# Optimization experiments

Measured on AMD Instinct MI355X. Metric: run time of the kernel, lower is better.

Reference implementation:

```python
import jax, jax.numpy as jnp
import numpy as np
import math

N_HEAD = 16
HEAD_QKV = 1024  # total qkv width; head_dim = HEAD_QKV // N_HEAD
WM_DECAY_LENGTH = 2048
WM_DECAY_RATE = 1.0
WM_ECHOIC = 16


def decay_weight_matrix(n):
    # power_law decay, faithful to get_decay_weight_matrix
    dl = WM_DECAY_LENGTH - WM_ECHOIC + 1
    nums = jnp.linspace(0.0, 1.0, dl)
    decay_values = 1.0 - jnp.power(nums, 1.0 / (np.e * WM_DECAY_RATE))
    decay_values = jnp.concatenate([jnp.ones(WM_ECHOIC - 1), decay_values])  # [WM_DECAY_LENGTH]
    decay_values = decay_values[:n]
    idx = jnp.arange(n)[:, None] - jnp.arange(n)[None, :]  # [n,n], negative above diag
    mat = decay_values[jnp.clip(idx, 0, n - 1)]
    return jnp.tril(mat).astype(jnp.float32)


def setup_inputs() -> dict:
    key = jax.random.key(0)
    k1, k2, k3 = jax.random.split(key, 3)
    B, T, C = 2, 2048, 1024
    x = jax.random.normal(k1, (B, T, C), dtype=jnp.float32)
    W_attn = jax.random.normal(k2, (C, 3 * HEAD_QKV), dtype=jnp.float32) * (1.0 / math.sqrt(C))
    W_proj = jax.random.normal(k3, (HEAD_QKV, C), dtype=jnp.float32) * (1.0 / math.sqrt(HEAD_QKV))
    return {"x": x, "W_attn": W_attn, "W_proj": W_proj}


def reference(x, W_attn, W_proj):
    B, T, C = x.shape
    hd = HEAD_QKV // N_HEAD
    qkv = x @ W_attn  # [B,T,3*HEAD_QKV]
    q, k, v = jnp.split(qkv, 3, axis=-1)
    # [B,T,HQKV] -> [B,H,T,hd]
    q = q.reshape(B, T, N_HEAD, hd).transpose(0, 2, 1, 3)
    k = k.reshape(B, T, N_HEAD, hd).transpose(0, 2, 1, 3)
    v = v.reshape(B, T, N_HEAD, hd).transpose(0, 2, 1, 3)
    att = jnp.einsum('bhqd,bhkd->bhqk', q, k) * (1.0 / math.sqrt(hd))
    causal = jnp.tril(jnp.ones((T, T), dtype=bool))
    att = jnp.where(causal, att, -jnp.inf)
    att = jax.nn.softmax(att, axis=-1)
    att = att * decay_weight_matrix(T)  # post-softmax multiplicative decay
    y = jnp.einsum('bhqk,bhkd->bhqd', att, v)
    y = y.transpose(0, 2, 1, 3).reshape(B, T, HEAD_QKV)
    return y @ W_proj
```

## Files before the change

kernel.cpp:

```cpp
#include <hip/hip_runtime.h>
#include <math.h>

#define B_  2
#define T_  2048
#define C_  1024
#define NH_ 16
#define HD_ 64
#define N3_ 3072

typedef float f32x4 __attribute__((ext_vector_type(4)));
typedef short bf16x8 __attribute__((ext_vector_type(8)));
typedef unsigned short u16;
typedef float f32x4_base __attribute__((ext_vector_type(4)));
typedef f32x4_base __attribute__((aligned(4))) f32x4u;

#define QSCALE 0.18033688011112042f

#if __has_builtin(__builtin_amdgcn_exp2f)
#define EXP2(x) __builtin_amdgcn_exp2f(x)
#else
#define EXP2(x) exp2f(x)
#endif

__device__ __forceinline__ u16 f2bf(float x) {
  unsigned int u = __builtin_bit_cast(unsigned int, x);
  u += 0x7FFFu + ((u >> 16) & 1u);
  return (u16)(u >> 16);
}

__device__ __forceinline__ unsigned int cvt_pk_bf16(float lo, float hi) {
  unsigned int r;
  asm("v_cvt_pk_bf16_f32 %0, %1, %2" : "=v"(r) : "v"(lo), "v"(hi));
  return r;
}

#define GLD16(g, l) __builtin_amdgcn_global_load_lds( \
    (__attribute__((address_space(1))) void*)(g), \
    (__attribute__((address_space(3))) void*)(l), 16, 0, 0)

__global__ __launch_bounds__(256) void prep_kernel(
    const float* __restrict__ x, u16* __restrict__ xb,
    const float* __restrict__ Wa, u16* __restrict__ WaT,
    const float* __restrict__ Wp, u16* __restrict__ WpT,
    float* __restrict__ decR)
{
  __shared__ float tile[32][33];
  const int bid = blockIdx.x;
  const int tid = threadIdx.x;
  if (bid < 4096) {
    int i = (bid * 256 + tid) * 4;
    float4 v = *(const float4*)(x + i);
    ushort4 o;
    o.x = f2bf(v.x); o.y = f2bf(v.y); o.z = f2bf(v.z); o.w = f2bf(v.w);
    *(ushort4*)(xb + i) = o;
  } else if (bid < 8192) {
    const float* in; u16* out; int Cc, c0, r0;
    if (bid < 7168) {
      int t = bid - 4096;
      in = Wa; out = WaT; Cc = N3_;
      c0 = (t % 96) * 32; r0 = (t / 96) * 32;
    } else {
      int t = bid - 7168;
      in = Wp; out = WpT; Cc = C_;
      c0 = (t % 32) * 32; r0 = (t / 32) * 32;
    }
    int tx = tid & 31, ty = tid >> 5;
#pragma unroll
    for (int rr = ty; rr < 32; rr += 8)
      tile[rr][tx] = in[(size_t)(r0 + rr) * Cc + c0 + tx];
    __syncthreads();
#pragma unroll
    for (int rr = ty; rr < 32; rr += 8)
      out[(size_t)(c0 + rr) * 1024 + r0 + tx] = f2bf(tile[tx][rr]);
  } else {
    int j = (bid - 8192) * 256 + tid;
    if (j < 4352) {
      int d = 2047 - j;
      float v = 1.0f;
      if (d >= 15) v = 1.0f - powf((float)(d - 15) * (1.0f / 2032.0f), 0.36787944117144233f);
      decR[j] = v;
    }
  }
}

__global__ void __launch_bounds__(512, 1) gemm256_kernel(
    const u16* __restrict__ A, const u16* __restrict__ Bt,
    u16* __restrict__ Cq, u16* __restrict__ Vt,
    int M, int N, int K)
{
  extern __shared__ char lds[];
  const int tid = threadIdx.x;
  const int lane = tid & 63;
  const int wave = tid >> 6;
  const int wm = wave >> 2;
  const int wn = wave & 3;
  const int quad = lane >> 4;
  const int l15 = lane & 15;
  const int nxb = N >> 8;
  const int orig = blockIdx.x;
  const int cpx = (int)gridDim.x >> 3;
  const int wg = (orig & 7) * cpx + (orig >> 3);
  const int m0 = (wg / nxb) << 8;
  const int n0 = (wg % nxb) << 8;

  f32x4 acc[8][4] = {};

  const int abase = wm * 16384;
  const int bbase = 65536 + (wn >> 1) * 16384;
  const int brow0 = (wn & 1) * 64;

#define HSTAGE(arr, rowbase, tile, ldsoff)                                       \
  {                                                                              \
    _Pragma("unroll")                                                            \
    for (int p = 0; p < 2; ++p) {                                                \
      int chunk = p * 8192 + tid * 16;                                           \
      int row = chunk >> 7;                                                      \
      int colb = (chunk & 127) ^ ((row & 7) << 4);                               \
      GLD16((const char*)((arr) + (size_t)((rowbase) + row) * K + (size_t)(tile) * 64) + colb, \
            lds + (ldsoff) + chunk);                                             \
    }                                                                            \
  }

#define PHASE(mg, buf, BLOAD, WAIT, STAGE_STMT)                                  \
  {                                                                              \
    if (WAIT) asm volatile("s_waitcnt vmcnt(4)" ::: "memory");                   \
    __builtin_amdgcn_s_barrier();                                                \
    __builtin_amdgcn_sched_barrier(0);                                           \
    STAGE_STMT;                                                                  \
    if (BLOAD) {                                                                 \
      _Pragma("unroll")                                                          \
      for (int n = 0; n < 4; ++n) {                                              \
        int rl = brow0 + n * 16 + l15;                                           \
        int msk = (rl & 7) << 4;                                                 \
        bfr[n][0] = *(const bf16x8*)(lds + bbase + (buf) * 32768 + rl * 128 +    \
                                     ((quad * 16) ^ msk));                       \
        bfr[n][1] = *(const bf16x8*)(lds + bbase + (buf) * 32768 + rl * 128 +    \
                                     ((64 + quad * 16) ^ msk));                  \
      }                                                                          \
    }                                                                            \
    bf16x8 af[2][2];                                                             \
    _Pragma("unroll")                                                            \
    for (int mm = 0; mm < 2; ++mm) {                                             \
      int rl = (mg) * 32 + mm * 16 + l15;                                        \
      int msk = (rl & 7) << 4;                                                   \
      af[mm][0] = *(const bf16x8*)(lds + abase + (buf) * 32768 + rl * 128 +      \
                                   ((quad * 16) ^ msk));                         \
      af[mm][1] = *(const bf16x8*)(lds + abase + (buf) * 32768 + rl * 128 +      \
                                   ((64 + quad * 16) ^ msk));                    \
    }                                                                            \
    __builtin_amdgcn_s_setprio(1);                                               \
    _Pragma("unroll")                                                            \
    for (int mm = 0; mm < 2; ++mm)                                               \
      _Pragma("unroll")                                                          \
      for (int n = 0; n < 4; ++n) {                                              \
        acc[(mg) * 2 + mm][n] = __builtin_amdgcn_mfma_f32_16x16x32_bf16(         \
            af[mm][0], bfr[n][0], acc[(mg) * 2 + mm][n], 0, 0, 0);               \
        acc[(mg) * 2 + mm][n] = __builtin_amdgcn_mfma_f32_16x16x32_bf16(         \
            af[mm][1], bfr[n][1], acc[(mg) * 2 + mm][n], 0, 0, 0);               \
      }                                                                          \
    __builtin_amdgcn_s_setprio(0);                                               \
  }

  bf16x8 bfr[4][2];

  HSTAGE(Bt, n0 + 0,   0, 65536 + 0);
  HSTAGE(Bt, n0 + 128, 0, 65536 + 16384);
  HSTAGE(A,  m0 + 0,   0, 0);
  HSTAGE(A,  m0 + 128, 0, 16384);
  HSTAGE(Bt, n0 + 0,   1, 65536 + 32768);
  HSTAGE(Bt, n0 + 128, 1, 65536 + 32768 + 16384);

  const int nt = K >> 6;
  const int tm = nt - 1;
  for (int j = 0; j < nt / 2; ++j) {
    const int t1 = 2 * j + 1, t2 = (2 * j + 2) & tm, t3 = (2 * j + 3) & tm;
    PHASE(0, 0, true,  true,  HSTAGE(A, m0 + 0,   t1, 32768));
    PHASE(1, 0, false, false, HSTAGE(A, m0 + 128, t1, 32768 + 16384));
    PHASE(2, 0, false, false, HSTAGE(Bt, n0 + 0,   t2, 65536));
    PHASE(3, 0, false, false, HSTAGE(Bt, n0 + 128, t2, 65536 + 16384));
    PHASE(0, 1, true,  true,  HSTAGE(A, m0 + 0,   t2, 0));
    PHASE(1, 1, false, false, HSTAGE(A, m0 + 128, t2, 16384));
    PHASE(2, 1, false, false, HSTAGE(Bt, n0 + 0,   t3, 65536 + 32768));
    PHASE(3, 1, false, false, HSTAGE(Bt, n0 + 128, t3, 65536 + 32768 + 16384));
  }
#undef PHASE
#undef HSTAGE

#pragma unroll
  for (int m = 0; m < 8; ++m) {
    int grow0 = m0 + wm * 128 + m * 16 + quad * 4;
#pragma unroll
    for (int n = 0; n < 4; ++n) {
      int gcol = n0 + wn * 64 + n * 16 + l15;
      f32x4 v = acc[m][n];
      int bb = grow0 >> 11, tt0 = grow0 & 2047;
      int which = gcol >> 10, rem = gcol & 1023;
      int hh = rem >> 6, dd = rem & 63;
      if (which < 2) {
#pragma unroll
        for (int r = 0; r < 4; ++r) {
          float ov = (which == 0) ? v[r] * QSCALE : v[r];
          Cq[((size_t)(which * 32 + bb * 16 + hh) * 2048 + tt0 + r) * 64 + dd] = f2bf(ov);
        }
      } else {
        ushort4 o;
        o.x = f2bf(v[0]); o.y = f2bf(v[1]); o.z = f2bf(v[2]); o.w = f2bf(v[3]);
        *(ushort4*)(Vt + ((size_t)(bb * 16 + hh) * 64 + dd) * 2048 + tt0) = o;
      }
    }
  }
}

__global__ __launch_bounds__(256, 3) void gemm128_kernel(
    const u16* __restrict__ A, const u16* __restrict__ Bt,
    float* __restrict__ Cf, int M, int N, int K)
{
  __shared__ char lds[49152];
  const int lane = threadIdx.x & 63;
  const int wave = threadIdx.x >> 6;
  const int nxb = N >> 7;
  const int orig = blockIdx.x;
  const int cpx = (int)gridDim.x >> 3;
  const int wg = (orig & 7) * cpx + (orig >> 3);
  const int m0 = (wg / nxb) << 7;
  const int n0 = (wg % nxb) << 7;
  const int wm = wave >> 1, wn = wave & 1;

  f32x4 acc[4][4] = {};

#define GSTAGE(buf, k0)                                                          \
  {                                                                              \
    _Pragma("unroll")                                                            \
    for (int c = 0; c < 2; ++c) {                                                \
      int chunk = wave * 2048 + c * 1024;                                        \
      int row = (chunk >> 6) + (lane >> 2);                                      \
      int wb = ((lane & 3) << 4) ^ ((row & 3) << 4);                             \
      GLD16((const char*)(A  + (size_t)(m0 + row) * K + (k0)) + wb,              \
            lds + (buf) * 16384 + chunk);                                        \
      GLD16((const char*)(Bt + (size_t)(n0 + row) * K + (k0)) + wb,              \
            lds + (buf) * 16384 + 8192 + chunk);                                 \
    }                                                                            \
  }

  const int nk = K >> 5;
  GSTAGE(0, 0);
  GSTAGE(1, 32);
  __syncthreads();

  for (int i = 0; i < nk; ++i) {
    if (i + 1 < nk) asm volatile("s_waitcnt vmcnt(4)" ::: "memory");
    else            asm volatile("s_waitcnt vmcnt(0)" ::: "memory");
    __builtin_amdgcn_s_barrier();
    __builtin_amdgcn_sched_barrier(0);
    if (i + 2 < nk) GSTAGE((i + 2) % 3, (i + 2) * 32);

    const char* base = lds + (i % 3) * 16384;
    bf16x8 af[4], bfr[4];
#pragma unroll
    for (int m = 0; m < 4; ++m) {
      int row = wm * 64 + m * 16 + (lane & 15);
      int wb = ((lane >> 4) << 4) ^ ((row & 3) << 4);
      af[m] = *(const bf16x8*)(base + row * 64 + wb);
    }
#pragma unroll
    for (int n = 0; n < 4; ++n) {
      int row = wn * 64 + n * 16 + (lane & 15);
      int wb = ((lane >> 4) << 4) ^ ((row & 3) << 4);
      bfr[n] = *(const bf16x8*)(base + 8192 + row * 64 + wb);
    }
    __builtin_amdgcn_s_setprio(1);
#pragma unroll
    for (int m = 0; m < 4; ++m)
#pragma unroll
      for (int n = 0; n < 4; ++n)
        acc[m][n] = __builtin_amdgcn_mfma_f32_16x16x32_bf16(af[m], bfr[n], acc[m][n], 0, 0, 0);
    __builtin_amdgcn_s_setprio(0);
  }

#pragma unroll
  for (int m = 0; m < 4; ++m) {
    int grow0 = m0 + wm * 64 + m * 16 + ((lane >> 4) << 2);
#pragma unroll
    for (int n = 0; n < 4; ++n) {
      int gcol = n0 + wn * 64 + n * 16 + (lane & 15);
      f32x4 v = acc[m][n];
#pragma unroll
      for (int r = 0; r < 4; ++r)
        Cf[(size_t)(grow0 + r) * N + gcol] = v[r];
    }
  }
#undef GSTAGE
}

__global__ __launch_bounds__(256, 2) void attn_kernel(
    const u16* __restrict__ qkb, const u16* __restrict__ vtg,
    const float* __restrict__ decR, u16* __restrict__ yb)
{
  __shared__ char klds[2][8192];
  __shared__ char vlds[2][8192];
  __shared__ u16 plds[64 * 76];

  const int lane = threadIdx.x & 63;
  const int wave = threadIdx.x >> 6;
  const int quad = lane >> 4;
  const int l15 = lane & 15;
  const int orig = blockIdx.x;
  const int xcd = orig & 7;
  const int bh = xcd * 4 + ((orig >> 3) & 3);
  const int x = orig >> 5;
  const int qtA = x;
  const int qtB = 31 - x;
  const int b = bh >> 4, h = bh & 15;

  const u16* Q   = qkb + (size_t)bh * T_ * HD_;
  const u16* Kg  = qkb + (size_t)(32 + bh) * T_ * HD_;
  const u16* VTg = vtg + (size_t)bh * HD_ * T_;

  const int wrowB = qtB * 64 + wave * 16;
  const int wrowA = qtA * 64 + wave * 16;
  const int qB = wrowB + l15;
  const int qA = wrowA + l15;
  const float* dpB = decR + (2047 - qB + quad * 4);
  const float* dpA = decR + (2047 - qA + quad * 4);

  bf16x8 qaB[2], qaA[2];
  { const u16* qp = Q + (size_t)qB * HD_ + quad * 8;
    qaB[0] = *(const bf16x8*)qp; qaB[1] = *(const bf16x8*)(qp + 32); }
  { const u16* qp = Q + (size_t)qA * HD_ + quad * 8;
    qaA[0] = *(const bf16x8*)qp; qaA[1] = *(const bf16x8*)(qp + 32); }

  f32x4 accB[4] = {}, accA[4] = {};
  float lsumB = 0.0f, lsumA = 0.0f;

#define ASTAGE(buf, kt)                                                          \
  {                                                                              \
    _Pragma("unroll")                                                            \
    for (int c = 0; c < 2; ++c) {                                                \
      int chunk = wave * 2048 + c * 1024;                                        \
      int row = (chunk >> 7) + (lane >> 3);                                      \
      int wb = ((lane & 7) << 4) ^ ((row & 7) << 4);                             \
      GLD16((const char*)(Kg + (size_t)((kt) * 64 + row) * HD_) + wb,            \
            klds[buf] + chunk);                                                  \
      GLD16((const char*)(VTg + (size_t)row * T_ + (kt) * 64) + wb,              \
            vlds[buf] + chunk);                                                  \
    }                                                                            \
  }

  const int twoA1 = 2 * qtA + 1;

  f32x4 dc[4], dn[4];
#pragma unroll
  for (int f = 0; f < 4; ++f) dn[f] = *(const f32x4u*)(dpB + f * 16);
  ASTAGE(0, 0);
  __syncthreads();

  for (int u = 0; u < 33; ++u) {
    const int kt   = (u <= twoA1) ? (u >> 1) : (u - qtA - 1);
    const int selA = (u <= twoA1) ? (u & 1) : 0;
    const int cur  = kt & 1;

#pragma unroll
    for (int f = 0; f < 4; ++f) dc[f] = dn[f];
    {
      const int u1 = u + 1;
      const int kt1   = (u1 <= twoA1) ? (u1 >> 1) : (u1 - qtA - 1);
      const int selA1 = (u1 <= twoA1) ? (u1 & 1) : 0;
      const float* dnp = (selA1 ? dpA : dpB) + kt1 * 64;
#pragma unroll
      for (int f = 0; f < 4; ++f) dn[f] = *(const f32x4u*)(dnp + f * 16);
    }

    asm volatile("s_waitcnt vmcnt(4)" ::: "memory");
    __builtin_amdgcn_s_barrier();
    __builtin_amdgcn_sched_barrier(0);
    if (!selA && kt < qtB) ASTAGE(cur ^ 1, kt + 1);

    bf16x8 kf[4][2];
#pragma unroll
    for (int f = 0; f < 4; ++f) {
      int krow = f * 16 + l15;
      int base = krow * 128;
      int msk = (krow & 7) << 4;
      kf[f][0] = *(const bf16x8*)(klds[cur] + base + ((quad * 16) ^ msk));
      kf[f][1] = *(const bf16x8*)(klds[cur] + base + ((64 + quad * 16) ^ msk));
    }

    const bf16x8 q0 = selA ? qaA[0] : qaB[0];
    const bf16x8 q1 = selA ? qaA[1] : qaB[1];
    f32x4 s[4];
    __builtin_amdgcn_s_setprio(1);
#pragma unroll
    for (int f = 0; f < 4; ++f) {
      f32x4 t = {};
      t = __builtin_amdgcn_mfma_f32_16x16x32_bf16(kf[f][0], q0, t, 0, 0, 0);
      t = __builtin_amdgcn_mfma_f32_16x16x32_bf16(kf[f][1], q1, t, 0, 0, 0);
      s[f] = t;
    }
    __builtin_amdgcn_s_setprio(0);

    const int qtsel = selA ? qtA : qtB;
    if (kt == qtsel) {
      const int qsel = selA ? qA : qB;
#pragma unroll
      for (int f = 0; f < 4; ++f) {
        int key0 = kt * 64 + f * 16 + quad * 4;
#pragma unroll
        for (int r = 0; r < 4; ++r)
          if (key0 + r > qsel) s[f][r] = -1e30f;
      }
    }

    float ls = 0.0f;
#pragma unroll
    for (int f = 0; f < 4; ++f) {
      f32x4 p;
#pragma unroll
      for (int r = 0; r < 4; ++r) p[r] = EXP2(s[f][r]);
      ls += (p[0] + p[1]) + (p[2] + p[3]);
      unsigned int w0 = cvt_pk_bf16(p[0] * dc[f][0], p[1] * dc[f][1]);
      unsigned int w1 = cvt_pk_bf16(p[2] * dc[f][2], p[3] * dc[f][3]);
      uint2 wv; wv.x = w0; wv.y = w1;
      *(uint2*)(plds + (size_t)(wave * 16 + l15) * 76 + f * 16 + quad * 4) = wv;
    }
    if (selA) lsumA += ls; else lsumB += ls;

    bf16x8 vf[4][2];
#pragma unroll
    for (int n = 0; n < 4; ++n) {
      int vrow = n * 16 + l15;
      int mskv = (vrow & 7) << 4;
#pragma unroll
      for (int ks = 0; ks < 2; ++ks)
        vf[n][ks] = *(const bf16x8*)(vlds[cur] + vrow * 128 + ((ks * 64 + quad * 16) ^ mskv));
    }

    bf16x8 pa0 = *(const bf16x8*)(plds + (size_t)(wave * 16 + l15) * 76 + quad * 8);
    bf16x8 pa1 = *(const bf16x8*)(plds + (size_t)(wave * 16 + l15) * 76 + 32 + quad * 8);
    __builtin_amdgcn_s_setprio(1);
    if (selA) {
#pragma unroll
      for (int n = 0; n < 4; ++n) {
        accA[n] = __builtin_amdgcn_mfma_f32_16x16x32_bf16(pa0, vf[n][0], accA[n], 0, 0, 0);
        accA[n] = __builtin_amdgcn_mfma_f32_16x16x32_bf16(pa1, vf[n][1], accA[n], 0, 0, 0);
      }
    } else {
#pragma unroll
      for (int n = 0; n < 4; ++n) {
        accB[n] = __builtin_amdgcn_mfma_f32_16x16x32_bf16(pa0, vf[n][0], accB[n], 0, 0, 0);
        accB[n] = __builtin_amdgcn_mfma_f32_16x16x32_bf16(pa1, vf[n][1], accB[n], 0, 0, 0);
      }
    }
    __builtin_amdgcn_s_setprio(0);
  }
#undef ASTAGE

  lsumB += __shfl_xor(lsumB, 16); lsumB += __shfl_xor(lsumB, 32);
  lsumA += __shfl_xor(lsumA, 16); lsumA += __shfl_xor(lsumA, 32);
  float rB[4], rA[4];
#pragma unroll
  for (int r = 0; r < 4; ++r) {
    rB[r] = 1.0f / __shfl(lsumB, quad * 4 + r, 16);
    rA[r] = 1.0f / __shfl(lsumA, quad * 4 + r, 16);
  }
#pragma unroll
  for (int n = 0; n < 4; ++n) {
    int d = h * 64 + n * 16 + l15;
#pragma unroll
    for (int r = 0; r < 4; ++r) {
      int tB = wrowB + quad * 4 + r;
      int tA = wrowA + quad * 4 + r;
      yb[((size_t)b * T_ + tB) * 1024 + d] = f2bf(accB[n][r] * rB[r]);
      yb[((size_t)b * T_ + tA) * 1024 + d] = f2bf(accA[n][r] * rA[r]);
    }
  }
}

extern "C" void kernel_launch(void* const* d_in, const int* in_sizes, int n_in,
                              void* d_out, int out_size, void* d_ws, size_t ws_size,
                              hipStream_t stream) {
  const float* x  = (const float*)d_in[0];
  const float* Wa = (const float*)d_in[1];
  const float* Wp = (const float*)d_in[2];
  float* out = (float*)d_out;
  char* ws = (char*)d_ws;

  u16*   xb    = (u16*)(ws + 0);
  u16*   WaT   = (u16*)(ws + 8388608);
  u16*   WpT   = (u16*)(ws + 14680064);
  u16*   qkb   = (u16*)(ws + 16777216);
  float* decR  = (float*)(ws + 33554432);
  u16*   VT    = (u16*)(ws + 41943040);
  u16*   yb    = xb;

  hipFuncSetAttribute((const void*)gemm256_kernel,
                      hipFuncAttributeMaxDynamicSharedMemorySize, 131072);

  prep_kernel<<<8209, 256, 0, stream>>>(x, xb, Wa, WaT, Wp, WpT, decR);
  gemm256_kernel<<<192, 512, 131072, stream>>>(xb, WaT, qkb, VT, B_ * T_, N3_, C_);
  attn_kernel<<<512, 256, 0, stream>>>(qkb, VT, decR, yb);
  gemm128_kernel<<<256, 256, 0, stream>>>(yb, WpT, out, B_ * T_, 1024, 1024);
}
```

Baseline: 101.2 us.

## Drop LDS K/V staging in attention; one query tile per block, direct global loads

Attention blocks no longer pair two query tiles, and K/V tiles are no longer staged through double-buffered LDS with async copies. Each wave now reads K and V^T fragments straight from global memory (relying on L2/cache reuse across the four waves). The grid doubles to 1024 blocks with heavier-tiles-first ordering and launch bounds rise to 4 blocks per SM for more occupancy. The cost is redundant global/L2 traffic per wave, the loss of prefetch overlap, and per-block load imbalance no longer evened out by pairing.

```diff
diff --git a/kernel.cpp b/kernel.cpp
--- a/kernel.cpp
+++ b/kernel.cpp
@@ -292,12 +292,10 @@
 #undef GSTAGE
 }
 
-__global__ __launch_bounds__(256, 2) void attn_kernel(
+__global__ __launch_bounds__(256, 4) void attn_kernel(
     const u16* __restrict__ qkb, const u16* __restrict__ vtg,
     const float* __restrict__ decR, u16* __restrict__ yb)
 {
-  __shared__ char klds[2][8192];
-  __shared__ char vlds[2][8192];
   __shared__ u16 plds[64 * 76];
 
   const int lane = threadIdx.x & 63;
@@ -305,172 +303,109 @@
   const int quad = lane >> 4;
   const int l15 = lane & 15;
   const int orig = blockIdx.x;
-  const int xcd = orig & 7;
-  const int bh = xcd * 4 + ((orig >> 3) & 3);
-  const int x = orig >> 5;
-  const int qtA = x;
-  const int qtB = 31 - x;
+  const int x = orig & 31;
+  const int bh = ((x & 7) << 2) + (x >> 3);
+  const int g = orig >> 5;
+  const int j3 = g >> 3;
+  const int g0 = g & 7;
+  const int qt = (3 - j3) * 8 + ((j3 & 1) ? (7 - g0) : g0);
   const int b = bh >> 4, h = bh & 15;
 
   const u16* Q   = qkb + (size_t)bh * T_ * HD_;
   const u16* Kg  = qkb + (size_t)(32 + bh) * T_ * HD_;
   const u16* VTg = vtg + (size_t)bh * HD_ * T_;
 
-  const int wrowB = qtB * 64 + wave * 16;
-  const int wrowA = qtA * 64 + wave * 16;
-  const int qB = wrowB + l15;
-  const int qA = wrowA + l15;
-  const float* dpB = decR + (2047 - qB + quad * 4);
-  const float* dpA = decR + (2047 - qA + quad * 4);
-
-  bf16x8 qaB[2], qaA[2];
-  { const u16* qp = Q + (size_t)qB * HD_ + quad * 8;
-    qaB[0] = *(const bf16x8*)qp; qaB[1] = *(const bf16x8*)(qp + 32); }
-  { const u16* qp = Q + (size_t)qA * HD_ + quad * 8;
-    qaA[0] = *(const bf16x8*)qp; qaA[1] = *(const bf16x8*)(qp + 32); }
-
-  f32x4 accB[4] = {}, accA[4] = {};
-  float lsumB = 0.0f, lsumA = 0.0f;
-
-#define ASTAGE(buf, kt)                                                          \
-  {                                                                              \
-    _Pragma("unroll")                                                            \
-    for (int c = 0; c < 2; ++c) {                                                \
-      int chunk = wave * 2048 + c * 1024;                                        \
-      int row = (chunk >> 7) + (lane >> 3);                                      \
-      int wb = ((lane & 7) << 4) ^ ((row & 7) << 4);                             \
-      GLD16((const char*)(Kg + (size_t)((kt) * 64 + row) * HD_) + wb,            \
-            klds[buf] + chunk);                                                  \
-      GLD16((const char*)(VTg + (size_t)row * T_ + (kt) * 64) + wb,              \
-            vlds[buf] + chunk);                                                  \
-    }                                                                            \
-  }
-
-  const int twoA1 = 2 * qtA + 1;
-
-  f32x4 dc[4], dn[4];
-#pragma unroll
-  for (int f = 0; f < 4; ++f) dn[f] = *(const f32x4u*)(dpB + f * 16);
-  ASTAGE(0, 0);
-  __syncthreads();
-
-  for (int u = 0; u < 33; ++u) {
-    const int kt   = (u <= twoA1) ? (u >> 1) : (u - qtA - 1);
-    const int selA = (u <= twoA1) ? (u & 1) : 0;
-    const int cur  = kt & 1;
-
-#pragma unroll
-    for (int f = 0; f < 4; ++f) dc[f] = dn[f];
-    {
-      const int u1 = u + 1;
-      const int kt1   = (u1 <= twoA1) ? (u1 >> 1) : (u1 - qtA - 1);
-      const int selA1 = (u1 <= twoA1) ? (u1 & 1) : 0;
-      const float* dnp = (selA1 ? dpA : dpB) + kt1 * 64;
-#pragma unroll
-      for (int f = 0; f < 4; ++f) dn[f] = *(const f32x4u*)(dnp + f * 16);
-    }
-
-    asm volatile("s_waitcnt vmcnt(4)" ::: "memory");
-    __builtin_amdgcn_s_barrier();
-    __builtin_amdgcn_sched_barrier(0);
-    if (!selA && kt < qtB) ASTAGE(cur ^ 1, kt + 1);
-
+  const int wrow = qt * 64 + wave * 16;
+  const int q = wrow + l15;
+  const float* dp = decR + (2047 - q + quad * 4);
+
+  bf16x8 qa[2];
+  { const u16* qp = Q + (size_t)q * HD_ + quad * 8;
+    qa[0] = *(const bf16x8*)qp; qa[1] = *(const bf16x8*)(qp + 32); }
+
+  f32x4 acc[4] = {};
+  float lsum = 0.0f;
+
+  for (int kt = 0; kt <= qt; ++kt) {
+    const u16* Kt = Kg + (size_t)(kt * 64) * HD_;
     bf16x8 kf[4][2];
 #pragma unroll
     for (int f = 0; f < 4; ++f) {
-      int krow = f * 16 + l15;
-      int base = krow * 128;
-      int msk = (krow & 7) << 4;
-      kf[f][0] = *(const bf16x8*)(klds[cur] + base + ((quad * 16) ^ msk));
-      kf[f][1] = *(const bf16x8*)(klds[cur] + base + ((64 + quad * 16) ^ msk));
-    }
-
-    const bf16x8 q0 = selA ? qaA[0] : qaB[0];
-    const bf16x8 q1 = selA ? qaA[1] : qaB[1];
+      const u16* kp = Kt + (size_t)(f * 16 + l15) * HD_ + quad * 8;
+      kf[f][0] = *(const bf16x8*)(kp);
+      kf[f][1] = *(const bf16x8*)(kp + 32);
+    }
+
+    f32x4 dc[4];
+    const float* dk = dp + kt * 64;
+#pragma unroll
+    for (int f = 0; f < 4; ++f) dc[f] = *(const f32x4u*)(dk + f * 16);
+
     f32x4 s[4];
     __builtin_amdgcn_s_setprio(1);
 #pragma unroll
     for (int f = 0; f < 4; ++f) {
       f32x4 t = {};
-      t = __builtin_amdgcn_mfma_f32_16x16x32_bf16(kf[f][0], q0, t, 0, 0, 0);
-      t = __builtin_amdgcn_mfma_f32_16x16x32_bf16(kf[f][1], q1, t, 0, 0, 0);
+      t = __builtin_amdgcn_mfma_f32_16x16x32_bf16(kf[f][0], qa[0], t, 0, 0, 0);
+      t = __builtin_amdgcn_mfma_f32_16x16x32_bf16(kf[f][1], qa[1], t, 0, 0, 0);
       s[f] = t;
     }
     __builtin_amdgcn_s_setprio(0);
 
-    const int qtsel = selA ? qtA : qtB;
-    if (kt == qtsel) {
-      const int qsel = selA ? qA : qB;
+    if (kt == qt) {
 #pragma unroll
       for (int f = 0; f < 4; ++f) {
         int key0 = kt * 64 + f * 16 + quad * 4;
 #pragma unroll
         for (int r = 0; r < 4; ++r)
-          if (key0 + r > qsel) s[f][r] = -1e30f;
+          if (key0 + r > q) s[f][r] = -1e30f;
       }
     }
 
-    float ls = 0.0f;
 #pragma unroll
     for (int f = 0; f < 4; ++f) {
       f32x4 p;
 #pragma unroll
       for (int r = 0; r < 4; ++r) p[r] = EXP2(s[f][r]);
-      ls += (p[0] + p[1]) + (p[2] + p[3]);
+      lsum += (p[0] + p[1]) + (p[2] + p[3]);
       unsigned int w0 = cvt_pk_bf16(p[0] * dc[f][0], p[1] * dc[f][1]);
       unsigned int w1 = cvt_pk_bf16(p[2] * dc[f][2], p[3] * dc[f][3]);
       uint2 wv; wv.x = w0; wv.y = w1;
       *(uint2*)(plds + (size_t)(wave * 16 + l15) * 76 + f * 16 + quad * 4) = wv;
     }
-    if (selA) lsumA += ls; else lsumB += ls;
 
     bf16x8 vf[4][2];
 #pragma unroll
     for (int n = 0; n < 4; ++n) {
-      int vrow = n * 16 + l15;
-      int mskv = (vrow & 7) << 4;
+      const u16* vp = VTg + (size_t)(n * 16 + l15) * T_ + kt * 64 + quad * 8;
 #pragma unroll
       for (int ks = 0; ks < 2; ++ks)
-        vf[n][ks] = *(const bf16x8*)(vlds[cur] + vrow * 128 + ((ks * 64 + quad * 16) ^ mskv));
+        vf[n][ks] = *(const bf16x8*)(vp + ks * 32);
     }
 
     bf16x8 pa0 = *(const bf16x8*)(plds + (size_t)(wave * 16 + l15) * 76 + quad * 8);
     bf16x8 pa1 = *(const bf16x8*)(plds + (size_t)(wave * 16 + l15) * 76 + 32 + quad * 8);
     __builtin_amdgcn_s_setprio(1);
-    if (selA) {
-#pragma unroll
-      for (int n = 0; n < 4; ++n) {
-        accA[n] = __builtin_amdgcn_mfma_f32_16x16x32_bf16(pa0, vf[n][0], accA[n], 0, 0, 0);
-        accA[n] = __builtin_amdgcn_mfma_f32_16x16x32_bf16(pa1, vf[n][1], accA[n], 0, 0, 0);
-      }
-    } else {
-#pragma unroll
-      for (int n = 0; n < 4; ++n) {
-        accB[n] = __builtin_amdgcn_mfma_f32_16x16x32_bf16(pa0, vf[n][0], accB[n], 0, 0, 0);
-        accB[n] = __builtin_amdgcn_mfma_f32_16x16x32_bf16(pa1, vf[n][1], accB[n], 0, 0, 0);
-      }
+#pragma unroll
+    for (int n = 0; n < 4; ++n) {
+      acc[n] = __builtin_amdgcn_mfma_f32_16x16x32_bf16(pa0, vf[n][0], acc[n], 0, 0, 0);
+      acc[n] = __builtin_amdgcn_mfma_f32_16x16x32_bf16(pa1, vf[n][1], acc[n], 0, 0, 0);
     }
     __builtin_amdgcn_s_setprio(0);
   }
-#undef ASTAGE
-
-  lsumB += __shfl_xor(lsumB, 16); lsumB += __shfl_xor(lsumB, 32);
-  lsumA += __shfl_xor(lsumA, 16); lsumA += __shfl_xor(lsumA, 32);
-  float rB[4], rA[4];
-#pragma unroll
-  for (int r = 0; r < 4; ++r) {
-    rB[r] = 1.0f / __shfl(lsumB, quad * 4 + r, 16);
-    rA[r] = 1.0f / __shfl(lsumA, quad * 4 + r, 16);
-  }
+
+  lsum += __shfl_xor(lsum, 16); lsum += __shfl_xor(lsum, 32);
+  float rb[4];
+#pragma unroll
+  for (int r = 0; r < 4; ++r)
+    rb[r] = 1.0f / __shfl(lsum, quad * 4 + r, 16);
 #pragma unroll
   for (int n = 0; n < 4; ++n) {
     int d = h * 64 + n * 16 + l15;
 #pragma unroll
     for (int r = 0; r < 4; ++r) {
-      int tB = wrowB + quad * 4 + r;
-      int tA = wrowA + quad * 4 + r;
-      yb[((size_t)b * T_ + tB) * 1024 + d] = f2bf(accB[n][r] * rB[r]);
-      yb[((size_t)b * T_ + tA) * 1024 + d] = f2bf(accA[n][r] * rA[r]);
+      int t = wrow + quad * 4 + r;
+      yb[((size_t)b * T_ + t) * 1024 + d] = f2bf(acc[n][r] * rb[r]);
     }
   }
 }
@@ -497,6 +432,6 @@
 
   prep_kernel<<<8209, 256, 0, stream>>>(x, xb, Wa, WaT, Wp, WpT, decR);
   gemm256_kernel<<<192, 512, 131072, stream>>>(xb, WaT, qkb, VT, B_ * T_, N3_, C_);
-  attn_kernel<<<512, 256, 0, stream>>>(qkb, VT, decR, yb);
+  attn_kernel<<<1024, 256, 0, stream>>>(qkb, VT, decR, yb);
   gemm128_kernel<<<256, 256, 0, stream>>>(yb, WpT, out, B_ * T_, 1024, 1024);
 }
```

Result: slower. 192.3 us (+90.1%).
